# Kernel tuning notes

Hardware: AMD Instinct MI355X
Metric: run time of the kernel (lower is better)

Reference implementation:

```python
import jax, jax.numpy as jnp
import numpy as np

N_NODES = 120000  # n_entities + n_users
N_REL = 16
D = 64   # entity_dim
R = 64   # relation_dim
E = 1600000


def setup_inputs() -> dict:
    key = jax.random.key(0)
    k1, k2, k3, k4, k5, k6 = jax.random.split(key, 6)
    return {
        "entity_user_embed": jax.random.normal(k1, (N_NODES, D), dtype=jnp.float32) * 0.1,
        "relation_embed": jax.random.normal(k2, (N_REL, R), dtype=jnp.float32) * 0.1,
        "W_R": jax.random.normal(k3, (N_REL, D, R), dtype=jnp.float32) * 0.1,
        "edge_src": jax.random.randint(k4, (E,), 0, N_NODES, dtype=jnp.int32),
        "edge_dst": jax.random.randint(k5, (E,), 0, N_NODES, dtype=jnp.int32),
        "edge_type": jax.random.randint(k6, (E,), 0, N_REL, dtype=jnp.int32),
    }


def reference(entity_user_embed, relation_embed, W_R, edge_src, edge_dst, edge_type):
    n_nodes = entity_user_embed.shape[0]
    # Per-relation transform of every node embedding: [n_rel, n_nodes, R].
    # Equivalent to the per-relation edge loop: matmul(emb[id], W_R[r]).
    trans = jnp.einsum('nd,rdk->rnk', entity_user_embed, W_R)
    r_mul_t = trans[edge_type, edge_src]   # [E, R] (edges.src path)
    r_mul_h = trans[edge_type, edge_dst]   # [E, R] (edges.dst path)
    r_embed = relation_embed[edge_type]    # [E, R]
    # bmm([E,1,R], [E,R,1]) -> per-edge dot product
    att = jnp.sum(r_mul_t * jnp.tanh(r_mul_h + r_embed), axis=-1)  # [E]
    # edge softmax over incoming edges of each destination node
    att_max = jax.ops.segment_max(att, edge_dst, num_segments=n_nodes)
    ex = jnp.exp(att - att_max[edge_dst])
    denom = jax.ops.segment_sum(ex, edge_dst, num_segments=n_nodes)
    out = ex / denom[edge_dst]
    return out[:, None]  # [E, 1], matching squeeze(-1) of [E,1,1]
```

## Files before the change

### kernel.cpp

```cpp
#include <hip/hip_runtime.h>
#include <hip/hip_bf16.h>

#define D64 64
#define NREL 16
#define SCALE 32.0f
#define INV_SCALE 0.03125f

typedef __attribute__((ext_vector_type(8))) short bf16x8;
typedef __attribute__((ext_vector_type(4))) float f32x4;
typedef __attribute__((ext_vector_type(2))) float f32x2;

__device__ __forceinline__ float tanh_fast(float x) {
    float e = __expf(2.0f * x);
    return 1.0f - 2.0f / (e + 1.0f);
}

__device__ __forceinline__ float tanh_poly(float x) {
    x = fmaxf(-1.5f, fminf(1.5f, x));
    float u = x * x;
    float p = fmaf(u, -0.0182227f, 0.108952f);
    p = fmaf(u, p, -0.329139f);
    p = fmaf(u, p, 1.0f);
    return x * p;
}

__device__ __forceinline__ unsigned short f2b(float x) {
    __hip_bfloat16 h = __float2bfloat16(x);
    return *reinterpret_cast<unsigned short*>(&h);
}

__global__ void zero_denom_kernel(float* __restrict__ denom, int n) {
    int i = blockIdx.x * blockDim.x + threadIdx.x;
    if (i < n) denom[i] = 0.0f;
}

__global__ void prep_kernel(const float* __restrict__ WR, const float* __restrict__ rel,
                            unsigned short* __restrict__ Wt, float* __restrict__ relp) {
    int i = blockIdx.x * blockDim.x + threadIdx.x;
    if (i < NREL * D64 * D64) {
        int r = i >> 12, rem = i & 4095, c = rem >> 6, d = rem & 63;
        Wt[i] = f2b(WR[(r << 12) + (d << 6) + c]);
    }
    if (i < NREL * D64) {
        int t = i >> 6, kp = i & 63;
        int q = kp >> 4, m = (kp >> 2) & 3, g = kp & 3;
        relp[i] = rel[t * D64 + m * 16 + q * 4 + g];
    }
}

__global__ __launch_bounds__(256)
void trans_gemm_kernel(const float* __restrict__ emb,
                       const unsigned short* __restrict__ Wt,
                       uint4* __restrict__ trans,
                       int n_nodes) {
    __shared__ unsigned short lbuf[2][4096];
    const int tid  = threadIdx.x;
    const int lane = tid & 63;
    const int wid  = tid >> 6;
    const int col  = lane & 15;
    const int quad = lane >> 4;
    const int rbase = (blockIdx.x & 1) * 8;
    const int nodebase = (blockIdx.x >> 1) * 256 + wid * 64;

    const int c0 = tid, c1 = tid + 256;
    const int mt0 = c0 >> 7, q20 = (c0 >> 6) & 1, ln0 = c0 & 63;
    const int so0 = ((mt0 * 16 + (ln0 & 15)) << 6) + (q20 << 5) + ((ln0 >> 4) << 3);
    const int do0 = (mt0 << 10) + (q20 << 9) + (ln0 << 3);
    const int mt1 = c1 >> 7, q21 = (c1 >> 6) & 1, ln1 = c1 & 63;
    const int so1 = ((mt1 * 16 + (ln1 & 15)) << 6) + (q21 << 5) + ((ln1 >> 4) << 3);
    const int do1 = (mt1 << 10) + (q21 << 9) + (ln1 << 3);

    bf16x8 bfr[4][2];
    int nds[4];
    #pragma unroll
    for (int j = 0; j < 4; ++j) {
        int node = nodebase + j * 16 + col;
        nds[j] = node;
        int cn = node < n_nodes ? node : n_nodes - 1;
        const float* bp = emb + (size_t)cn * D64 + quad * 8;
        #pragma unroll
        for (int ks = 0; ks < 2; ++ks) {
            float4 v0 = *(const float4*)(bp + ks * 32);
            float4 v1 = *(const float4*)(bp + ks * 32 + 4);
            bfr[j][ks][0] = (short)f2b(v0.x); bfr[j][ks][1] = (short)f2b(v0.y);
            bfr[j][ks][2] = (short)f2b(v0.z); bfr[j][ks][3] = (short)f2b(v0.w);
            bfr[j][ks][4] = (short)f2b(v1.x); bfr[j][ks][5] = (short)f2b(v1.y);
            bfr[j][ks][6] = (short)f2b(v1.z); bfr[j][ks][7] = (short)f2b(v1.w);
        }
    }

    {
        const unsigned short* w = Wt + (rbase << 12);
        bf16x8 s0 = *(const bf16x8*)(w + so0);
        bf16x8 s1 = *(const bf16x8*)(w + so1);
        *(bf16x8*)(&lbuf[0][do0]) = s0;
        *(bf16x8*)(&lbuf[0][do1]) = s1;
    }
    __syncthreads();

    #pragma unroll 1
    for (int rr = 0; rr < 8; ++rr) {
        const int r = rbase + rr;
        const int cur = rr & 1;

        bf16x8 n0, n1;
        if (rr < 7) {
            const unsigned short* wn = Wt + ((r + 1) << 12);
            n0 = *(const bf16x8*)(wn + so0);
            n1 = *(const bf16x8*)(wn + so1);
        }

        const unsigned short* lb = lbuf[cur];
        f32x4 acc[4][4];
        #pragma unroll
        for (int mt = 0; mt < 4; ++mt) {
            bf16x8 a0 = *(const bf16x8*)(lb + (mt << 10) + (lane << 3));
            bf16x8 a1 = *(const bf16x8*)(lb + (mt << 10) + 512 + (lane << 3));
            #pragma unroll
            for (int j = 0; j < 4; ++j) {
                f32x4 c = {0.f, 0.f, 0.f, 0.f};
                c = __builtin_amdgcn_mfma_f32_16x16x32_bf16(a0, bfr[j][0], c, 0, 0, 0);
                c = __builtin_amdgcn_mfma_f32_16x16x32_bf16(a1, bfr[j][1], c, 0, 0, 0);
                acc[mt][j] = c;
            }
        }

        #pragma unroll
        for (int j = 0; j < 4; ++j) {
            if (nds[j] < n_nodes) {
                uint4 pk;
                unsigned p;
                p = __builtin_amdgcn_cvt_pk_fp8_f32(acc[0][j][0] * SCALE, acc[0][j][1] * SCALE, 0, false);
                p = __builtin_amdgcn_cvt_pk_fp8_f32(acc[0][j][2] * SCALE, acc[0][j][3] * SCALE, p, true);
                pk.x = p;
                p = __builtin_amdgcn_cvt_pk_fp8_f32(acc[1][j][0] * SCALE, acc[1][j][1] * SCALE, 0, false);
                p = __builtin_amdgcn_cvt_pk_fp8_f32(acc[1][j][2] * SCALE, acc[1][j][3] * SCALE, p, true);
                pk.y = p;
                p = __builtin_amdgcn_cvt_pk_fp8_f32(acc[2][j][0] * SCALE, acc[2][j][1] * SCALE, 0, false);
                p = __builtin_amdgcn_cvt_pk_fp8_f32(acc[2][j][2] * SCALE, acc[2][j][3] * SCALE, p, true);
                pk.z = p;
                p = __builtin_amdgcn_cvt_pk_fp8_f32(acc[3][j][0] * SCALE, acc[3][j][1] * SCALE, 0, false);
                p = __builtin_amdgcn_cvt_pk_fp8_f32(acc[3][j][2] * SCALE, acc[3][j][3] * SCALE, p, true);
                pk.w = p;
                trans[((size_t)r * n_nodes + nds[j]) * 4 + quad] = pk;
            }
        }

        if (rr < 7) {
            *(bf16x8*)(&lbuf[1 - cur][do0]) = n0;
            *(bf16x8*)(&lbuf[1 - cur][do1]) = n1;
            __syncthreads();
        }
    }
}

__device__ __forceinline__ void term4(unsigned ut, unsigned uh, float4 r, float& acc) {
    f32x2 tlo = __builtin_amdgcn_cvt_pk_f32_fp8(ut, false);
    f32x2 thi = __builtin_amdgcn_cvt_pk_f32_fp8(ut, true);
    f32x2 hlo = __builtin_amdgcn_cvt_pk_f32_fp8(uh, false);
    f32x2 hhi = __builtin_amdgcn_cvt_pk_f32_fp8(uh, true);
    acc += tlo[0] * tanh_poly(fmaf(hlo[0], INV_SCALE, r.x));
    acc += tlo[1] * tanh_poly(fmaf(hlo[1], INV_SCALE, r.y));
    acc += thi[0] * tanh_poly(fmaf(hhi[0], INV_SCALE, r.z));
    acc += thi[1] * tanh_poly(fmaf(hhi[1], INV_SCALE, r.w));
}

__global__ __launch_bounds__(256)
void edge_kernel(const unsigned* __restrict__ trans,
                 const float* __restrict__ relp,
                 const int* __restrict__ esrc, const int* __restrict__ edst,
                 const int* __restrict__ etype,
                 float* __restrict__ out, float* __restrict__ denom,
                 int E, int n_nodes) {
    int e0 = blockIdx.x * 512 + threadIdx.x;
    int e1 = e0 + 256;
    bool v0 = e0 < E, v1 = e1 < E;
    int i0 = v0 ? e0 : 0;
    int i1 = v1 ? e1 : 0;
    int t0 = etype[i0], s0 = esrc[i0], d0 = edst[i0];
    int t1 = etype[i1], s1 = esrc[i1], d1 = edst[i1];

    const uint4* pt0 = (const uint4*)(trans + ((size_t)t0 * n_nodes + s0) * 16);
    const uint4* ph0 = (const uint4*)(trans + ((size_t)t0 * n_nodes + d0) * 16);
    const uint4* pt1 = (const uint4*)(trans + ((size_t)t1 * n_nodes + s1) * 16);
    const uint4* ph1 = (const uint4*)(trans + ((size_t)t1 * n_nodes + d1) * 16);

    uint4 T0[4], H0[4], T1[4], H1[4];
    #pragma unroll
    for (int c4 = 0; c4 < 4; ++c4) {
        T0[c4] = pt0[c4]; H0[c4] = ph0[c4];
        T1[c4] = pt1[c4]; H1[c4] = ph1[c4];
    }

    const float4* pr0 = (const float4*)(relp + t0 * D64);
    const float4* pr1 = (const float4*)(relp + t1 * D64);
    float a0 = 0.f, a1 = 0.f;
    #pragma unroll
    for (int c4 = 0; c4 < 4; ++c4) {
        term4(T0[c4].x, H0[c4].x, pr0[c4 * 4 + 0], a0);
        term4(T1[c4].x, H1[c4].x, pr1[c4 * 4 + 0], a1);
        term4(T0[c4].y, H0[c4].y, pr0[c4 * 4 + 1], a0);
        term4(T1[c4].y, H1[c4].y, pr1[c4 * 4 + 1], a1);
        term4(T0[c4].z, H0[c4].z, pr0[c4 * 4 + 2], a0);
        term4(T1[c4].z, H1[c4].z, pr1[c4 * 4 + 2], a1);
        term4(T0[c4].w, H0[c4].w, pr0[c4 * 4 + 3], a0);
        term4(T1[c4].w, H1[c4].w, pr1[c4 * 4 + 3], a1);
    }
    if (v0) {
        float ex = __expf(a0 * INV_SCALE);
        out[e0] = ex;
        atomicAdd(&denom[d0], ex);
    }
    if (v1) {
        float ex = __expf(a1 * INV_SCALE);
        out[e1] = ex;
        atomicAdd(&denom[d1], ex);
    }
}

__global__ void normalize_kernel(float* __restrict__ out,
                                 const float* __restrict__ denom,
                                 const int* __restrict__ edst, int E) {
    int e = blockIdx.x * blockDim.x + threadIdx.x;
    if (e < E) out[e] = out[e] / denom[edst[e]];
}

__global__ __launch_bounds__(256)
void edge_att_fallback(const float* __restrict__ emb, const float* __restrict__ rel,
                       const float* __restrict__ WR, const int* __restrict__ esrc,
                       const int* __restrict__ edst, const int* __restrict__ etype,
                       float* __restrict__ exbuf, float* __restrict__ denom,
                       int E, int chunkSize) {
    const int type = blockIdx.x & 15;
    const int c    = blockIdx.x >> 4;
    const int lane = threadIdx.x & 63;
    const int wid  = threadIdx.x >> 6;
    long base0 = (long)c * (long)chunkSize;
    long cend  = base0 + chunkSize;
    if (cend > E) cend = E;
    if (base0 >= cend) return;
    int per = (chunkSize + 3) >> 2;
    long wbeg = base0 + (long)wid * per;
    long wend = wbeg + per;
    if (wend > cend) wend = cend;
    if (wbeg >= wend) return;
    float w[D64];
    const float* Wt = WR + (size_t)type * D64 * D64;
    #pragma unroll
    for (int d = 0; d < D64; ++d) w[d] = Wt[d * D64 + lane];
    const float rk = rel[type * D64 + lane];
    for (long s0 = wbeg; s0 < wend; s0 += 64) {
        long e = s0 + lane;
        int ty = -1, sv = 0, dv = 0;
        if (e < wend) { ty = etype[e]; sv = esrc[e]; dv = edst[e]; }
        unsigned long long m = __ballot(ty == type);
        while (m) {
            int b = __builtin_ctzll(m);
            m &= m - 1;
            int sn = __builtin_amdgcn_readlane(sv, b);
            int dn = __builtin_amdgcn_readlane(dv, b);
            const float4* es4 = (const float4*)(emb + (size_t)sn * D64);
            const float4* ed4 = (const float4*)(emb + (size_t)dn * D64);
            float t0 = 0.f, t1 = 0.f, t2 = 0.f, t3 = 0.f;
            float h0 = 0.f, h1 = 0.f, h2 = 0.f, h3 = 0.f;
            #pragma unroll
            for (int i = 0; i < D64 / 4; ++i) {
                float4 a = es4[i]; float4 b4 = ed4[i];
                t0 = fmaf(a.x, w[4*i+0], t0); t1 = fmaf(a.y, w[4*i+1], t1);
                t2 = fmaf(a.z, w[4*i+2], t2); t3 = fmaf(a.w, w[4*i+3], t3);
                h0 = fmaf(b4.x, w[4*i+0], h0); h1 = fmaf(b4.y, w[4*i+1], h1);
                h2 = fmaf(b4.z, w[4*i+2], h2); h3 = fmaf(b4.w, w[4*i+3], h3);
            }
            float t = (t0 + t1) + (t2 + t3);
            float h = (h0 + h1) + (h2 + h3);
            float p = t * tanh_fast(h + rk);
            #pragma unroll
            for (int off = 32; off > 0; off >>= 1) p += __shfl_xor(p, off);
            if (lane == 0) {
                float ex = __expf(p);
                exbuf[s0 + b] = ex;
                atomicAdd(&denom[dn], ex);
            }
        }
    }
}

__global__ void normalize_fallback(float* __restrict__ out,
                                   const float* __restrict__ denom,
                                   const int* __restrict__ edst, int E) {
    int e = blockIdx.x * blockDim.x + threadIdx.x;
    if (e < E) out[e] = out[e] / denom[edst[e]];
}

extern "C" void kernel_launch(void* const* d_in, const int* in_sizes, int n_in,
                              void* d_out, int out_size, void* d_ws, size_t ws_size,
                              hipStream_t stream) {
    const float* emb  = (const float*)d_in[0];
    const float* rel  = (const float*)d_in[1];
    const float* WR   = (const float*)d_in[2];
    const int*   esrc = (const int*)d_in[3];
    const int*   edst = (const int*)d_in[4];
    const int*   ety  = (const int*)d_in[5];

    const int E       = in_sizes[3];
    const int n_nodes = in_sizes[0] / D64;
    float* out = (float*)d_out;

    size_t transB = (size_t)NREL * n_nodes * D64;
    size_t off_trans = 0;
    size_t off_wt    = (off_trans + transB + 255) & ~(size_t)255;
    size_t off_rel   = (off_wt + (size_t)NREL * D64 * D64 * 2 + 255) & ~(size_t)255;
    size_t off_den   = (off_rel + (size_t)NREL * D64 * 4 + 255) & ~(size_t)255;
    size_t need      = off_den + (size_t)n_nodes * sizeof(float);

    if (ws_size >= need) {
        uint4*          trans = (uint4*)((char*)d_ws + off_trans);
        unsigned short* Wt    = (unsigned short*)((char*)d_ws + off_wt);
        float*          relp  = (float*)((char*)d_ws + off_rel);
        float*          denom = (float*)((char*)d_ws + off_den);

        prep_kernel<<<(NREL * D64 * D64 + 255) / 256, 256, 0, stream>>>(WR, rel, Wt, relp);
        zero_denom_kernel<<<(n_nodes + 255) / 256, 256, 0, stream>>>(denom, n_nodes);
        trans_gemm_kernel<<<((n_nodes + 255) / 256) * 2, 256, 0, stream>>>(emb, Wt, trans, n_nodes);
        edge_kernel<<<(E + 511) / 512, 256, 0, stream>>>((const unsigned*)trans, relp,
                                                         esrc, edst, ety,
                                                         out, denom, E, n_nodes);
        normalize_kernel<<<(E + 255) / 256, 256, 0, stream>>>(out, denom, edst, E);
    } else {
        float* denom = (float*)d_ws;
        zero_denom_kernel<<<(n_nodes + 255) / 256, 256, 0, stream>>>(denom, n_nodes);
        const int NCHUNK = 256;
        int chunk = (E + NCHUNK - 1) / NCHUNK;
        edge_att_fallback<<<16 * NCHUNK, 256, 0, stream>>>(emb, rel, WR, esrc, edst, ety,
                                                           out, denom, E, chunk);
        normalize_fallback<<<(E + 255) / 256, 256, 0, stream>>>(out, denom, edst, E);
    }
}
```

Measured before the change: 243.4 us.

## Fuse denom zeroing into prep, preload all relation weights, fold scale into W

```diff
diff --git a/kernel.cpp b/kernel.cpp
--- a/kernel.cpp
+++ b/kernel.cpp
@@ -29,23 +29,20 @@
     return *reinterpret_cast<unsigned short*>(&h);
 }
 
-__global__ void zero_denom_kernel(float* __restrict__ denom, int n) {
-    int i = blockIdx.x * blockDim.x + threadIdx.x;
-    if (i < n) denom[i] = 0.0f;
-}
-
 __global__ void prep_kernel(const float* __restrict__ WR, const float* __restrict__ rel,
-                            unsigned short* __restrict__ Wt, float* __restrict__ relp) {
+                            unsigned short* __restrict__ Wt, float* __restrict__ relp,
+                            float* __restrict__ denom, int n_nodes) {
     int i = blockIdx.x * blockDim.x + threadIdx.x;
     if (i < NREL * D64 * D64) {
         int r = i >> 12, rem = i & 4095, c = rem >> 6, d = rem & 63;
-        Wt[i] = f2b(WR[(r << 12) + (d << 6) + c]);
+        Wt[i] = f2b(WR[(r << 12) + (d << 6) + c] * SCALE);
     }
     if (i < NREL * D64) {
         int t = i >> 6, kp = i & 63;
         int q = kp >> 4, m = (kp >> 2) & 3, g = kp & 3;
         relp[i] = rel[t * D64 + m * 16 + q * 4 + g];
     }
+    if (i < n_nodes) denom[i] = 0.0f;
 }
 
 __global__ __launch_bounds__(256)
@@ -53,7 +50,7 @@
                        const unsigned short* __restrict__ Wt,
                        uint4* __restrict__ trans,
                        int n_nodes) {
-    __shared__ unsigned short lbuf[2][4096];
+    __shared__ unsigned short lbuf[8 * 4096];
     const int tid  = threadIdx.x;
     const int lane = tid & 63;
     const int wid  = tid >> 6;
@@ -62,13 +59,15 @@
     const int rbase = (blockIdx.x & 1) * 8;
     const int nodebase = (blockIdx.x >> 1) * 256 + wid * 64;
 
-    const int c0 = tid, c1 = tid + 256;
-    const int mt0 = c0 >> 7, q20 = (c0 >> 6) & 1, ln0 = c0 & 63;
-    const int so0 = ((mt0 * 16 + (ln0 & 15)) << 6) + (q20 << 5) + ((ln0 >> 4) << 3);
-    const int do0 = (mt0 << 10) + (q20 << 9) + (ln0 << 3);
-    const int mt1 = c1 >> 7, q21 = (c1 >> 6) & 1, ln1 = c1 & 63;
-    const int so1 = ((mt1 * 16 + (ln1 & 15)) << 6) + (q21 << 5) + ((ln1 >> 4) << 3);
-    const int do1 = (mt1 << 10) + (q21 << 9) + (ln1 << 3);
+    const unsigned short* wbase = Wt + (rbase << 12);
+    #pragma unroll
+    for (int k = 0; k < 16; ++k) {
+        int c = tid + k * 256;
+        int rr = c >> 9, cc = c & 511;
+        int mt = cc >> 7, q2 = (cc >> 6) & 1, ln = cc & 63;
+        int so = (rr << 12) + ((mt * 16 + (ln & 15)) << 6) + (q2 << 5) + ((ln >> 4) << 3);
+        *(bf16x8*)(&lbuf[c << 3]) = *(const bf16x8*)(wbase + so);
+    }
 
     bf16x8 bfr[4][2];
     int nds[4];
@@ -89,28 +88,12 @@
         }
     }
 
-    {
-        const unsigned short* w = Wt + (rbase << 12);
-        bf16x8 s0 = *(const bf16x8*)(w + so0);
-        bf16x8 s1 = *(const bf16x8*)(w + so1);
-        *(bf16x8*)(&lbuf[0][do0]) = s0;
-        *(bf16x8*)(&lbuf[0][do1]) = s1;
-    }
     __syncthreads();
 
     #pragma unroll 1
     for (int rr = 0; rr < 8; ++rr) {
         const int r = rbase + rr;
-        const int cur = rr & 1;
-
-        bf16x8 n0, n1;
-        if (rr < 7) {
-            const unsigned short* wn = Wt + ((r + 1) << 12);
-            n0 = *(const bf16x8*)(wn + so0);
-            n1 = *(const bf16x8*)(wn + so1);
-        }
-
-        const unsigned short* lb = lbuf[cur];
+        const unsigned short* lb = lbuf + (rr << 12);
         f32x4 acc[4][4];
         #pragma unroll
         for (int mt = 0; mt < 4; ++mt) {
@@ -124,32 +107,25 @@
                 acc[mt][j] = c;
             }
         }
-
         #pragma unroll
         for (int j = 0; j < 4; ++j) {
             if (nds[j] < n_nodes) {
                 uint4 pk;
                 unsigned p;
-                p = __builtin_amdgcn_cvt_pk_fp8_f32(acc[0][j][0] * SCALE, acc[0][j][1] * SCALE, 0, false);
-                p = __builtin_amdgcn_cvt_pk_fp8_f32(acc[0][j][2] * SCALE, acc[0][j][3] * SCALE, p, true);
+                p = __builtin_amdgcn_cvt_pk_fp8_f32(acc[0][j][0], acc[0][j][1], 0, false);
+                p = __builtin_amdgcn_cvt_pk_fp8_f32(acc[0][j][2], acc[0][j][3], p, true);
                 pk.x = p;
-                p = __builtin_amdgcn_cvt_pk_fp8_f32(acc[1][j][0] * SCALE, acc[1][j][1] * SCALE, 0, false);
-                p = __builtin_amdgcn_cvt_pk_fp8_f32(acc[1][j][2] * SCALE, acc[1][j][3] * SCALE, p, true);
+                p = __builtin_amdgcn_cvt_pk_fp8_f32(acc[1][j][0], acc[1][j][1], 0, false);
+                p = __builtin_amdgcn_cvt_pk_fp8_f32(acc[1][j][2], acc[1][j][3], p, true);
                 pk.y = p;
-                p = __builtin_amdgcn_cvt_pk_fp8_f32(acc[2][j][0] * SCALE, acc[2][j][1] * SCALE, 0, false);
-                p = __builtin_amdgcn_cvt_pk_fp8_f32(acc[2][j][2] * SCALE, acc[2][j][3] * SCALE, p, true);
+                p = __builtin_amdgcn_cvt_pk_fp8_f32(acc[2][j][0], acc[2][j][1], 0, false);
+                p = __builtin_amdgcn_cvt_pk_fp8_f32(acc[2][j][2], acc[2][j][3], p, true);
                 pk.z = p;
-                p = __builtin_amdgcn_cvt_pk_fp8_f32(acc[3][j][0] * SCALE, acc[3][j][1] * SCALE, 0, false);
-                p = __builtin_amdgcn_cvt_pk_fp8_f32(acc[3][j][2] * SCALE, acc[3][j][3] * SCALE, p, true);
+                p = __builtin_amdgcn_cvt_pk_fp8_f32(acc[3][j][0], acc[3][j][1], 0, false);
+                p = __builtin_amdgcn_cvt_pk_fp8_f32(acc[3][j][2], acc[3][j][3], p, true);
                 pk.w = p;
                 trans[((size_t)r * n_nodes + nds[j]) * 4 + quad] = pk;
             }
-        }
-
-        if (rr < 7) {
-            *(bf16x8*)(&lbuf[1 - cur][do0]) = n0;
-            *(bf16x8*)(&lbuf[1 - cur][do1]) = n1;
-            __syncthreads();
         }
     }
 }
@@ -223,6 +199,11 @@
                                  const int* __restrict__ edst, int E) {
     int e = blockIdx.x * blockDim.x + threadIdx.x;
     if (e < E) out[e] = out[e] / denom[edst[e]];
+}
+
+__global__ void zero_denom_kernel(float* __restrict__ denom, int n) {
+    int i = blockIdx.x * blockDim.x + threadIdx.x;
+    if (i < n) denom[i] = 0.0f;
 }
 
 __global__ __launch_bounds__(256)
@@ -319,8 +300,9 @@
         float*          relp  = (float*)((char*)d_ws + off_rel);
         float*          denom = (float*)((char*)d_ws + off_den);
 
-        prep_kernel<<<(NREL * D64 * D64 + 255) / 256, 256, 0, stream>>>(WR, rel, Wt, relp);
-        zero_denom_kernel<<<(n_nodes + 255) / 256, 256, 0, stream>>>(denom, n_nodes);
+        int prepN = n_nodes > NREL * D64 * D64 ? n_nodes : NREL * D64 * D64;
+        prep_kernel<<<(prepN + 255) / 256, 256, 0, stream>>>(WR, rel, Wt, relp,
+                                                             denom, n_nodes);
         trans_gemm_kernel<<<((n_nodes + 255) / 256) * 2, 256, 0, stream>>>(emb, Wt, trans, n_nodes);
         edge_kernel<<<(E + 511) / 512, 256, 0, stream>>>((const unsigned*)trans, relp,
                                                          esrc, edst, ety,
```

After: 241.3 us. Within noise of the previous version (-0.9%).
